# Performance work log

Hardware: AMD Instinct MI355X
Metric: run time of the kernel (lower is better)

Reference implementation:

```python
import jax, jax.numpy as jnp
import numpy as np

DIM = 128
NUM_HEADS = 4
WIN = (7, 7)
N = WIN[0] * WIN[1]
HEAD_DIM = DIM // NUM_HEADS
SCALE = HEAD_DIM ** -0.5
NW = 64


def _relative_position_index():
    coords_h = np.arange(WIN[0])
    coords_w = np.arange(WIN[1])
    coords = np.stack(np.meshgrid(coords_h, coords_w, indexing='ij'))  # [2, Wh, Ww]
    cf = coords.reshape(2, -1)
    rel = cf[:, :, None] - cf[:, None, :]  # [2, N, N]
    rel = rel.transpose(1, 2, 0)
    rel[:, :, 0] += WIN[0] - 1
    rel[:, :, 1] += WIN[1] - 1
    rel[:, :, 0] *= 2 * WIN[1] - 1
    return rel.sum(-1).astype(np.int32)  # [N, N]


def setup_inputs() -> dict:
    key = jax.random.key(0)
    ks = jax.random.split(key, 8)
    B_ = 4096  # num_windows_per_image * image_batch = 64 * 64
    x = jax.random.normal(ks[0], (B_, N, DIM), dtype=jnp.float32)
    mask = jax.random.normal(ks[1], (NW, N, N), dtype=jnp.float32)  # additive shift mask
    qkv_w = jax.random.normal(ks[2], (DIM, 3 * DIM), dtype=jnp.float32) * (DIM ** -0.5)
    qkv_b = jnp.zeros((3 * DIM,), dtype=jnp.float32)
    proj_w = jax.random.normal(ks[3], (DIM, DIM), dtype=jnp.float32) * (DIM ** -0.5)
    proj_b = jnp.zeros((DIM,), dtype=jnp.float32)
    rel_bias_table = jax.random.normal(ks[4], ((2 * WIN[0] - 1) * (2 * WIN[1] - 1), NUM_HEADS), dtype=jnp.float32) * 0.02
    rel_index = jnp.asarray(_relative_position_index())
    return {"x": x, "mask": mask, "qkv_w": qkv_w, "qkv_b": qkv_b,
            "proj_w": proj_w, "proj_b": proj_b,
            "rel_bias_table": rel_bias_table, "rel_index": rel_index}


def reference(x, mask, qkv_w, qkv_b, proj_w, proj_b, rel_bias_table, rel_index):
    B_, n, C = x.shape
    # qkv projection -> [3, B_, H, N, hd]
    qkv = (x @ qkv_w + qkv_b).reshape(B_, n, 3, NUM_HEADS, HEAD_DIM)
    qkv = jnp.transpose(qkv, (2, 0, 3, 1, 4))
    q, k, v = qkv[0], qkv[1], qkv[2]
    attn = jnp.einsum('bhnd,bhmd->bhnm', q * SCALE, k)  # [B_, H, N, N]
    # gathered relative position bias: [N, N, H] -> [H, N, N]
    bias = rel_bias_table[rel_index.reshape(-1)].reshape(n, n, NUM_HEADS)
    attn = attn + jnp.transpose(bias, (2, 0, 1))[None]
    # additive shift mask, broadcast over image batch
    nW = mask.shape[0]
    attn = attn.reshape(-1, nW, NUM_HEADS, n, n) + mask[None, :, None]
    attn = attn.reshape(-1, NUM_HEADS, n, n)
    attn = jax.nn.softmax(attn, axis=-1)
    out = jnp.einsum('bhnm,bhmd->bnhd', attn, v).reshape(B_, n, C)
    return out @ proj_w + proj_b
```

## Files before the change

### kernel.cpp

```cpp
#include <hip/hip_runtime.h>

#define NWIN 49
#define DIM  128
#define NH   4
#define HD   32
#define SCALE 0.17677669529663687f

using short8 = __attribute__((ext_vector_type(8))) short;
using f32x4  = __attribute__((ext_vector_type(4))) float;

union Frag { uint4 u; short8 s; };

static __device__ __forceinline__ short8 ld8(const unsigned short* p) {
    Frag fr; fr.u = *(const uint4*)p; return fr.s;
}
static __device__ __forceinline__ unsigned short f2bf(float f) {
    union { float f; unsigned i; } v; v.f = f;
    unsigned r = v.i + 0x7fffu + ((v.i >> 16) & 1u);
    return (unsigned short)(r >> 16);
}

__global__ __launch_bounds__(256) void prep_kernel(
    const float* __restrict__ qkv_w,
    const float* __restrict__ proj_w,
    const float* __restrict__ mask,
    const float* __restrict__ bias_tab,
    const int*   __restrict__ rel_index,
    unsigned short* __restrict__ wqkvT,
    unsigned short* __restrict__ projT,
    float*          __restrict__ BM)
{
    int tid = blockIdx.x * 256 + threadIdx.x;
    if (tid < 49152) {
        int n = tid >> 7, k = tid & 127;
        wqkvT[tid] = f2bf(qkv_w[k * 384 + n]);
    } else if (tid < 65536) {
        int t2 = tid - 49152;
        int n = t2 >> 7, k = t2 & 127;
        projT[t2] = f2bf(proj_w[k * 128 + n]);
    } else if (tid < 65536 + 64 * NH * 2401) {
        int idx = tid - 65536;
        int wh = idx / 2401, ij = idx % 2401;
        int wm = wh >> 2, h = wh & 3;
        BM[idx] = mask[wm * 2401 + ij] + bias_tab[rel_index[ij] * NH + h];
    }
}

#define XS_STRIDE 136
#define WPOOL_OFF 13328
#define WPOOL_SZ  12448
#define QH_OFF    4608
#define KH_OFF    8528
#define PS_OFF    4608
#define POOL_SZ   65168

__global__ __launch_bounds__(512) void winattn_kernel(
    const float* __restrict__ x,
    const float* __restrict__ qkv_b,
    const float* __restrict__ proj_b,
    const unsigned short* __restrict__ wqkvT,
    const unsigned short* __restrict__ projT,
    const float* __restrict__ BM,
    float*       __restrict__ out)
{
    __shared__ __align__(16) char pool[POOL_SZ];
    unsigned short* XS = (unsigned short*)pool;

    const int b = blockIdx.x;
    const int t = threadIdx.x;
    const int w = t >> 6;
    const int lane = t & 63;
    const int q = lane >> 4;
    const int l16 = lane & 15;
    const int wm = b & 63;

    for (int c = t; c < NWIN * 16; c += 512) {
        const int row = c >> 4, g = c & 15;
        const float4* src = (const float4*)(x + (size_t)b * (NWIN * DIM) + row * DIM + g * 8);
        float4 f0 = src[0], f1 = src[1];
        uint4 p;
        p.x = (unsigned)f2bf(f0.x) | ((unsigned)f2bf(f0.y) << 16);
        p.y = (unsigned)f2bf(f0.z) | ((unsigned)f2bf(f0.w) << 16);
        p.z = (unsigned)f2bf(f1.x) | ((unsigned)f2bf(f1.y) << 16);
        p.w = (unsigned)f2bf(f1.z) | ((unsigned)f2bf(f1.w) << 16);
        *(uint4*)(XS + row * XS_STRIDE + g * 8) = p;
    }
    __syncthreads();

    {
        const int hb = w & 3;
        const int mt0 = w >> 2;
        char* wpb = pool + WPOOL_OFF + hb * WPOOL_SZ;
        unsigned short* VTb = (unsigned short*)wpb;
        unsigned short* QHb = (unsigned short*)(wpb + QH_OFF);
        unsigned short* KHb = (unsigned short*)(wpb + KH_OFF);

        short8 af[2][4];
        #pragma unroll
        for (int mti = 0; mti < 2; ++mti) {
            const int mt = mt0 + 2 * mti;
            #pragma unroll
            for (int ks = 0; ks < 4; ++ks)
                af[mti][ks] = ld8(XS + (mt * 16 + l16) * XS_STRIDE + ks * 32 + q * 8);
        }
        #pragma unroll
        for (int sn = 0; sn < 6; ++sn) {
            const int s = sn >> 1, nn = sn & 1;
            const int colbase = s * 128 + hb * 32 + nn * 16;
            short8 bfr[4];
            #pragma unroll
            for (int ks = 0; ks < 4; ++ks)
                bfr[ks] = ld8(wqkvT + (size_t)(colbase + l16) * 128 + ks * 32 + q * 8);
            const float bias = qkv_b[colbase + l16];
            const int cl = nn * 16 + l16;
            #pragma unroll
            for (int mti = 0; mti < 2; ++mti) {
                const int mt = mt0 + 2 * mti;
                f32x4 acc = {0.f, 0.f, 0.f, 0.f};
                #pragma unroll
                for (int ks = 0; ks < 4; ++ks)
                    acc = __builtin_amdgcn_mfma_f32_16x16x32_bf16(af[mti][ks], bfr[ks], acc, 0, 0, 0);
                #pragma unroll
                for (int r = 0; r < 4; ++r) {
                    const int row = mt * 16 + q * 4 + r;
                    const float val = acc[r] + bias;
                    if (s == 0)      { if (row < NWIN) QHb[row * 40 + cl] = f2bf(val * SCALE); }
                    else if (s == 1) { if (row < NWIN) KHb[row * 40 + cl] = f2bf(val); }
                    else             VTb[cl * 72 + row] = f2bf(val);
                }
            }
        }
    }
    __syncthreads();

    const int h = w >> 1, mh = w & 1;
    char* wp = pool + WPOOL_OFF + h * WPOOL_SZ;
    unsigned short* VT = (unsigned short*)wp;
    unsigned short* QH = (unsigned short*)(wp + QH_OFF);
    unsigned short* KH = (unsigned short*)(wp + KH_OFF);
    unsigned short* PS = (unsigned short*)(wp + PS_OFF);

    float sv[2][4][4];
    {
        short8 kf[4];
        #pragma unroll
        for (int nt = 0; nt < 4; ++nt)
            kf[nt] = ld8(KH + (nt * 16 + l16) * 40 + q * 8);
        #pragma unroll
        for (int mti = 0; mti < 2; ++mti) {
            const int mt = 2 * mh + mti;
            short8 a = ld8(QH + (mt * 16 + l16) * 40 + q * 8);
            #pragma unroll
            for (int nt = 0; nt < 4; ++nt) {
                f32x4 acc = {0.f, 0.f, 0.f, 0.f};
                acc = __builtin_amdgcn_mfma_f32_16x16x32_bf16(a, kf[nt], acc, 0, 0, 0);
                #pragma unroll
                for (int r = 0; r < 4; ++r) sv[mti][nt][r] = acc[r];
            }
        }
    }
    {
        const float* bm = BM + (size_t)(wm * NH + h) * 2401;
        #pragma unroll
        for (int mti = 0; mti < 2; ++mti)
            #pragma unroll
            for (int r = 0; r < 4; ++r) {
                const int i = (2 * mh + mti) * 16 + q * 4 + r;
                const float* bmr = bm + i * 49;
                #pragma unroll
                for (int nt = 0; nt < 4; ++nt) {
                    const int j = nt * 16 + l16;
                    if (j >= NWIN)      sv[mti][nt][r] = -1e30f;
                    else if (i < NWIN)  sv[mti][nt][r] += bmr[j];
                }
            }
    }
    #pragma unroll
    for (int mti = 0; mti < 2; ++mti)
        #pragma unroll
        for (int r = 0; r < 4; ++r) {
            float m = fmaxf(fmaxf(sv[mti][0][r], sv[mti][1][r]),
                            fmaxf(sv[mti][2][r], sv[mti][3][r]));
            m = fmaxf(m, __shfl_xor(m, 1));
            m = fmaxf(m, __shfl_xor(m, 2));
            m = fmaxf(m, __shfl_xor(m, 4));
            m = fmaxf(m, __shfl_xor(m, 8));
            float sum = 0.f;
            #pragma unroll
            for (int nt = 0; nt < 4; ++nt) {
                float e = __expf(sv[mti][nt][r] - m);
                sv[mti][nt][r] = e;
                sum += e;
            }
            sum += __shfl_xor(sum, 1);
            sum += __shfl_xor(sum, 2);
            sum += __shfl_xor(sum, 4);
            sum += __shfl_xor(sum, 8);
            const float rs = 1.f / sum;
            #pragma unroll
            for (int nt = 0; nt < 4; ++nt) sv[mti][nt][r] *= rs;
        }

    __syncthreads();

    #pragma unroll
    for (int mti = 0; mti < 2; ++mti)
        #pragma unroll
        for (int r = 0; r < 4; ++r) {
            const int i = (2 * mh + mti) * 16 + q * 4 + r;
            if (i < NWIN) {
                #pragma unroll
                for (int nt = 0; nt < 4; ++nt)
                    PS[i * 72 + nt * 16 + l16] = f2bf(sv[mti][nt][r]);
            }
        }

    #pragma unroll
    for (int nt2 = 0; nt2 < 2; ++nt2) {
        short8 bv0 = ld8(VT + (nt2 * 16 + l16) * 72 + q * 8);
        short8 bv1 = ld8(VT + (nt2 * 16 + l16) * 72 + 32 + q * 8);
        #pragma unroll
        for (int mti = 0; mti < 2; ++mti) {
            const int mt = 2 * mh + mti;
            f32x4 acc = {0.f, 0.f, 0.f, 0.f};
            acc = __builtin_amdgcn_mfma_f32_16x16x32_bf16(
                ld8(PS + (mt * 16 + l16) * 72 + q * 8), bv0, acc, 0, 0, 0);
            acc = __builtin_amdgcn_mfma_f32_16x16x32_bf16(
                ld8(PS + (mt * 16 + l16) * 72 + 32 + q * 8), bv1, acc, 0, 0, 0);
            #pragma unroll
            for (int r = 0; r < 4; ++r) {
                const int row = mt * 16 + q * 4 + r;
                if (row < NWIN)
                    XS[row * XS_STRIDE + h * 32 + nt2 * 16 + l16] = f2bf(acc[r]);
            }
        }
    }
    __syncthreads();

    {
        const int nt = w;
        short8 bfr[4];
        #pragma unroll
        for (int ks = 0; ks < 4; ++ks)
            bfr[ks] = ld8(projT + (size_t)(nt * 16 + l16) * 128 + ks * 32 + q * 8);
        const int col = nt * 16 + l16;
        const float pb = proj_b[col];
        #pragma unroll
        for (int mt = 0; mt < 4; ++mt) {
            f32x4 acc = {0.f, 0.f, 0.f, 0.f};
            const unsigned short* arow = XS + (mt * 16 + l16) * XS_STRIDE + q * 8;
            #pragma unroll
            for (int ks = 0; ks < 4; ++ks)
                acc = __builtin_amdgcn_mfma_f32_16x16x32_bf16(ld8(arow + ks * 32),
                                                              bfr[ks], acc, 0, 0, 0);
            #pragma unroll
            for (int r = 0; r < 4; ++r) {
                const int row = mt * 16 + q * 4 + r;
                if (row < NWIN)
                    out[(size_t)b * (NWIN * DIM) + row * 128 + col] = acc[r] + pb;
            }
        }
    }
}

extern "C" void kernel_launch(void* const* d_in, const int* in_sizes, int n_in,
                              void* d_out, int out_size, void* d_ws, size_t ws_size,
                              hipStream_t stream) {
    const int B = in_sizes[0] / (NWIN * DIM);
    unsigned short* wqkvT = (unsigned short*)d_ws;
    unsigned short* projT = (unsigned short*)((char*)d_ws + 98304);
    float*          BM    = (float*)((char*)d_ws + 131072);

    prep_kernel<<<2657, 256, 0, stream>>>(
        (const float*)d_in[2],
        (const float*)d_in[4],
        (const float*)d_in[1],
        (const float*)d_in[6],
        (const int*)d_in[7],
        wqkvT, projT, BM);

    winattn_kernel<<<B, 512, 0, stream>>>(
        (const float*)d_in[0],
        (const float*)d_in[3],
        (const float*)d_in[5],
        wqkvT, projT, BM,
        (float*)d_out);
}
```

Before: 327.4 us.

## Swizzle LDS layouts with XOR, clamp padded rows, use DPP row reductions

Replaces the padded-stride shared-memory layouts for X, Q, K, V^T and P with unpadded layouts that XOR-swizzle the byte offset by the row index. This is meant to avoid LDS bank conflicts while shrinking the LDS footprint, which could allow more blocks per CU. Out-of-range rows in the last tile are clamped to row 48 instead of reading padding. V^T stores become packed 4-element writes, and the softmax row max and sum use DPP lane moves instead of shuffles.

```diff
diff --git a/kernel.cpp b/kernel.cpp
--- a/kernel.cpp
+++ b/kernel.cpp
@@ -7,17 +7,39 @@
 #define SCALE 0.17677669529663687f
 
 using short8 = __attribute__((ext_vector_type(8))) short;
+using us4    = __attribute__((ext_vector_type(4))) unsigned short;
 using f32x4  = __attribute__((ext_vector_type(4))) float;
 
 union Frag { uint4 u; short8 s; };
 
-static __device__ __forceinline__ short8 ld8(const unsigned short* p) {
+static __device__ __forceinline__ short8 ld8p(const void* p) {
     Frag fr; fr.u = *(const uint4*)p; return fr.s;
 }
 static __device__ __forceinline__ unsigned short f2bf(float f) {
     union { float f; unsigned i; } v; v.f = f;
     unsigned r = v.i + 0x7fffu + ((v.i >> 16) & 1u);
     return (unsigned short)(r >> 16);
+}
+
+template <int CTRL>
+static __device__ __forceinline__ float dppf(float x) {
+    int v = __float_as_int(x);
+    v = __builtin_amdgcn_update_dpp(v, v, CTRL, 0xF, 0xF, false);
+    return __int_as_float(v);
+}
+static __device__ __forceinline__ float rowmax16(float m) {
+    m = fmaxf(m, dppf<0xB1>(m));
+    m = fmaxf(m, dppf<0x4E>(m));
+    m = fmaxf(m, dppf<0x124>(m));
+    m = fmaxf(m, dppf<0x128>(m));
+    return m;
+}
+static __device__ __forceinline__ float rowsum16(float s) {
+    s += dppf<0xB1>(s);
+    s += dppf<0x4E>(s);
+    s += dppf<0x124>(s);
+    s += dppf<0x128>(s);
+    return s;
 }
 
 __global__ __launch_bounds__(256) void prep_kernel(
@@ -46,13 +68,12 @@
     }
 }
 
-#define XS_STRIDE 136
-#define WPOOL_OFF 13328
-#define WPOOL_SZ  12448
-#define QH_OFF    4608
-#define KH_OFF    8528
-#define PS_OFF    4608
-#define POOL_SZ   65168
+#define SWZ(r)  (((r) & 7) << 4)
+#define HP_B   12544
+#define HP_SZ  10368
+#define KH_B   3136
+#define VT_B   6272
+#define LDS_SZ 54016
 
 __global__ __launch_bounds__(512) void winattn_kernel(
     const float* __restrict__ x,
@@ -63,8 +84,7 @@
     const float* __restrict__ BM,
     float*       __restrict__ out)
 {
-    __shared__ __align__(16) char pool[POOL_SZ];
-    unsigned short* XS = (unsigned short*)pool;
+    __shared__ __align__(16) char pool[LDS_SZ];
 
     const int b = blockIdx.x;
     const int t = threadIdx.x;
@@ -83,25 +103,24 @@
         p.y = (unsigned)f2bf(f0.z) | ((unsigned)f2bf(f0.w) << 16);
         p.z = (unsigned)f2bf(f1.x) | ((unsigned)f2bf(f1.y) << 16);
         p.w = (unsigned)f2bf(f1.z) | ((unsigned)f2bf(f1.w) << 16);
-        *(uint4*)(XS + row * XS_STRIDE + g * 8) = p;
+        *(uint4*)(pool + ((row * 256 + g * 16) ^ SWZ(row))) = p;
     }
     __syncthreads();
 
     {
         const int hb = w & 3;
         const int mt0 = w >> 2;
-        char* wpb = pool + WPOOL_OFF + hb * WPOOL_SZ;
-        unsigned short* VTb = (unsigned short*)wpb;
-        unsigned short* QHb = (unsigned short*)(wpb + QH_OFF);
-        unsigned short* KHb = (unsigned short*)(wpb + KH_OFF);
+        char* hp = pool + HP_B + hb * HP_SZ;
 
         short8 af[2][4];
         #pragma unroll
         for (int mti = 0; mti < 2; ++mti) {
             const int mt = mt0 + 2 * mti;
+            int rr = mt * 16 + l16;
+            if (mt == 3) rr = rr > 48 ? 48 : rr;
             #pragma unroll
             for (int ks = 0; ks < 4; ++ks)
-                af[mti][ks] = ld8(XS + (mt * 16 + l16) * XS_STRIDE + ks * 32 + q * 8);
+                af[mti][ks] = ld8p(pool + ((rr * 256 + ks * 64 + q * 16) ^ SWZ(rr)));
         }
         #pragma unroll
         for (int sn = 0; sn < 6; ++sn) {
@@ -110,7 +129,7 @@
             short8 bfr[4];
             #pragma unroll
             for (int ks = 0; ks < 4; ++ks)
-                bfr[ks] = ld8(wqkvT + (size_t)(colbase + l16) * 128 + ks * 32 + q * 8);
+                bfr[ks] = ld8p(wqkvT + (size_t)(colbase + l16) * 128 + ks * 32 + q * 8);
             const float bias = qkv_b[colbase + l16];
             const int cl = nn * 16 + l16;
             #pragma unroll
@@ -120,13 +139,23 @@
                 #pragma unroll
                 for (int ks = 0; ks < 4; ++ks)
                     acc = __builtin_amdgcn_mfma_f32_16x16x32_bf16(af[mti][ks], bfr[ks], acc, 0, 0, 0);
-                #pragma unroll
-                for (int r = 0; r < 4; ++r) {
-                    const int row = mt * 16 + q * 4 + r;
-                    const float val = acc[r] + bias;
-                    if (s == 0)      { if (row < NWIN) QHb[row * 40 + cl] = f2bf(val * SCALE); }
-                    else if (s == 1) { if (row < NWIN) KHb[row * 40 + cl] = f2bf(val); }
-                    else             VTb[cl * 72 + row] = f2bf(val);
+                if (s == 2) {
+                    us4 pk;
+                    #pragma unroll
+                    for (int r = 0; r < 4; ++r) pk[r] = f2bf(acc[r] + bias);
+                    *(us4*)(hp + VT_B + ((cl * 128 + mt * 32 + q * 8) ^ SWZ(cl))) = pk;
+                } else {
+                    #pragma unroll
+                    for (int r = 0; r < 4; ++r) {
+                        const int row = mt * 16 + q * 4 + r;
+                        if (row < NWIN) {
+                            const float val = acc[r] + bias;
+                            if (s == 0)
+                                *(unsigned short*)(hp + ((row * 64 + cl * 2) ^ SWZ(row))) = f2bf(val * SCALE);
+                            else
+                                *(unsigned short*)(hp + KH_B + ((row * 64 + cl * 2) ^ SWZ(row))) = f2bf(val);
+                        }
+                    }
                 }
             }
         }
@@ -134,22 +163,23 @@
     __syncthreads();
 
     const int h = w >> 1, mh = w & 1;
-    char* wp = pool + WPOOL_OFF + h * WPOOL_SZ;
-    unsigned short* VT = (unsigned short*)wp;
-    unsigned short* QH = (unsigned short*)(wp + QH_OFF);
-    unsigned short* KH = (unsigned short*)(wp + KH_OFF);
-    unsigned short* PS = (unsigned short*)(wp + PS_OFF);
+    char* hp = pool + HP_B + h * HP_SZ;
 
     float sv[2][4][4];
     {
         short8 kf[4];
         #pragma unroll
-        for (int nt = 0; nt < 4; ++nt)
-            kf[nt] = ld8(KH + (nt * 16 + l16) * 40 + q * 8);
+        for (int nt = 0; nt < 4; ++nt) {
+            int rn = nt * 16 + l16;
+            if (nt == 3) rn = rn > 48 ? 48 : rn;
+            kf[nt] = ld8p(hp + KH_B + ((rn * 64 + q * 16) ^ SWZ(rn)));
+        }
         #pragma unroll
         for (int mti = 0; mti < 2; ++mti) {
             const int mt = 2 * mh + mti;
-            short8 a = ld8(QH + (mt * 16 + l16) * 40 + q * 8);
+            int rr = mt * 16 + l16;
+            if (mt == 3) rr = rr > 48 ? 48 : rr;
+            short8 a = ld8p(hp + ((rr * 64 + q * 16) ^ SWZ(rr)));
             #pragma unroll
             for (int nt = 0; nt < 4; ++nt) {
                 f32x4 acc = {0.f, 0.f, 0.f, 0.f};
@@ -181,10 +211,7 @@
         for (int r = 0; r < 4; ++r) {
             float m = fmaxf(fmaxf(sv[mti][0][r], sv[mti][1][r]),
                             fmaxf(sv[mti][2][r], sv[mti][3][r]));
-            m = fmaxf(m, __shfl_xor(m, 1));
-            m = fmaxf(m, __shfl_xor(m, 2));
-            m = fmaxf(m, __shfl_xor(m, 4));
-            m = fmaxf(m, __shfl_xor(m, 8));
+            m = rowmax16(m);
             float sum = 0.f;
             #pragma unroll
             for (int nt = 0; nt < 4; ++nt) {
@@ -192,10 +219,7 @@
                 sv[mti][nt][r] = e;
                 sum += e;
             }
-            sum += __shfl_xor(sum, 1);
-            sum += __shfl_xor(sum, 2);
-            sum += __shfl_xor(sum, 4);
-            sum += __shfl_xor(sum, 8);
+            sum = rowsum16(sum);
             const float rs = 1.f / sum;
             #pragma unroll
             for (int nt = 0; nt < 4; ++nt) sv[mti][nt][r] *= rs;
@@ -211,27 +235,30 @@
             if (i < NWIN) {
                 #pragma unroll
                 for (int nt = 0; nt < 4; ++nt)
-                    PS[i * 72 + nt * 16 + l16] = f2bf(sv[mti][nt][r]);
+                    *(unsigned short*)(hp + ((i * 128 + (nt * 16 + l16) * 2) ^ SWZ(i))) = f2bf(sv[mti][nt][r]);
             }
         }
 
     #pragma unroll
     for (int nt2 = 0; nt2 < 2; ++nt2) {
-        short8 bv0 = ld8(VT + (nt2 * 16 + l16) * 72 + q * 8);
-        short8 bv1 = ld8(VT + (nt2 * 16 + l16) * 72 + 32 + q * 8);
+        const int d = nt2 * 16 + l16;
+        short8 bv0 = ld8p(hp + VT_B + ((d * 128 + q * 16) ^ SWZ(d)));
+        short8 bv1 = ld8p(hp + VT_B + ((d * 128 + 64 + q * 16) ^ SWZ(d)));
         #pragma unroll
         for (int mti = 0; mti < 2; ++mti) {
             const int mt = 2 * mh + mti;
+            int rr = mt * 16 + l16;
+            if (mt == 3) rr = rr > 48 ? 48 : rr;
             f32x4 acc = {0.f, 0.f, 0.f, 0.f};
             acc = __builtin_amdgcn_mfma_f32_16x16x32_bf16(
-                ld8(PS + (mt * 16 + l16) * 72 + q * 8), bv0, acc, 0, 0, 0);
+                ld8p(hp + ((rr * 128 + q * 16) ^ SWZ(rr))), bv0, acc, 0, 0, 0);
             acc = __builtin_amdgcn_mfma_f32_16x16x32_bf16(
-                ld8(PS + (mt * 16 + l16) * 72 + 32 + q * 8), bv1, acc, 0, 0, 0);
+                ld8p(hp + ((rr * 128 + 64 + q * 16) ^ SWZ(rr))), bv1, acc, 0, 0, 0);
             #pragma unroll
             for (int r = 0; r < 4; ++r) {
                 const int row = mt * 16 + q * 4 + r;
                 if (row < NWIN)
-                    XS[row * XS_STRIDE + h * 32 + nt2 * 16 + l16] = f2bf(acc[r]);
+                    *(unsigned short*)(pool + ((row * 256 + (h * 32 + nt2 * 16 + l16) * 2) ^ SWZ(row))) = f2bf(acc[r]);
             }
         }
     }
@@ -242,17 +269,18 @@
         short8 bfr[4];
         #pragma unroll
         for (int ks = 0; ks < 4; ++ks)
-            bfr[ks] = ld8(projT + (size_t)(nt * 16 + l16) * 128 + ks * 32 + q * 8);
+            bfr[ks] = ld8p(projT + (size_t)(nt * 16 + l16) * 128 + ks * 32 + q * 8);
         const int col = nt * 16 + l16;
         const float pb = proj_b[col];
         #pragma unroll
         for (int mt = 0; mt < 4; ++mt) {
+            int rr = mt * 16 + l16;
+            if (mt == 3) rr = rr > 48 ? 48 : rr;
             f32x4 acc = {0.f, 0.f, 0.f, 0.f};
-            const unsigned short* arow = XS + (mt * 16 + l16) * XS_STRIDE + q * 8;
             #pragma unroll
             for (int ks = 0; ks < 4; ++ks)
-                acc = __builtin_amdgcn_mfma_f32_16x16x32_bf16(ld8(arow + ks * 32),
-                                                              bfr[ks], acc, 0, 0, 0);
+                acc = __builtin_amdgcn_mfma_f32_16x16x32_bf16(
+                    ld8p(pool + ((rr * 256 + ks * 64 + q * 16) ^ SWZ(rr))), bfr[ks], acc, 0, 0, 0);
             #pragma unroll
             for (int r = 0; r < 4; ++r) {
                 const int row = mt * 16 + q * 4 + r;
```

New measurement: 328.5 us. No clear change (+0.3%).
